# Kernel optimization log

Hardware: AMD Instinct MI355X
Metric: run time of the kernel (lower is better)

The kernel has to match this reference:

```python
import jax, jax.numpy as jnp
import numpy as np

S, N, C = 16384, 2048, 8  # n_samples, n_channels, n_components

def setup_inputs() -> dict:
    key = jax.random.key(0)
    k1, k2, k3, k4 = jax.random.split(key, 4)
    return {
        "inputs": jax.random.uniform(k1, (S, N), dtype=jnp.float32),
        "components": jax.random.uniform(k2, (C, N), dtype=jnp.float32),
        "contributions": jax.random.uniform(k3, (S, C), dtype=jnp.float32),
        "shift": jax.random.normal(k4, (S, C), dtype=jnp.float32) * 3.0,
    }

def reference(inputs, components, contributions, shift):
    # fit_shift=True branch. The original builds k_matrix[i,j] = j - i and
    # coeff[i,j] = clip(1 - |shift - (j - i)|, 0, 1), then dots with the
    # component. That is exactly linear interpolation of component at
    # position i + shift, with zero padding outside [0, N-1].
    n_samples, n_channels = inputs.shape
    n_comp = components.shape[0]
    i = jnp.arange(n_channels, dtype=shift.dtype)
    pos = i[None, None, :] + shift[:, :, None]            # [S, C, N]
    j0f = jnp.floor(pos)
    frac = pos - j0f                                      # in [0, 1)
    j0 = j0f.astype(jnp.int32)
    j1 = j0 + 1
    cidx = jnp.arange(n_comp)[None, :, None]              # broadcast over [S, C, N]
    g0 = components[cidx, jnp.clip(j0, 0, n_channels - 1)]
    g1 = components[cidx, jnp.clip(j1, 0, n_channels - 1)]
    v0 = ((j0 >= 0) & (j0 < n_channels)).astype(components.dtype)
    v1 = ((j1 >= 0) & (j1 < n_channels)).astype(components.dtype)
    shifted = g0 * (1.0 - frac) * v0 + g1 * frac * v1     # [S, C, N] shifted components
    # scale by per-sample contributions and sum over components
    return jnp.einsum('scn,sc->sn', shifted, contributions)
```

## Files before the change

kernel.cpp:

```cpp
#include <hip/hip_runtime.h>
#include <hip/hip_fp16.h>


namespace {
constexpr int kS     = 16384;
constexpr int kN     = 2048;
constexpr int kC     = 8;
constexpr int kM     = 16;
constexpr int kBlock = 256;
constexpr int kPadH  = 32;
constexpr int kUnits = 1057;
constexpr int kRowStride = 1192;

__device__ __forceinline__ int swz(int u) { return u + (u >> 3); }

__global__ __launch_bounds__(kBlock, 4)
void smf_kernel(const float* __restrict__ comps,
                const float* __restrict__ contrib,
                const float* __restrict__ shift,
                float* __restrict__ out)
{
    __shared__ uint32_t ldsU[kC * kRowStride];

    const int tid = threadIdx.x;

    for (int c = 0; c < kC; ++c) {
        const float* src = comps + c * kN;
        uint32_t* dst = ldsU + c * kRowStride;
        for (int u = tid; u < kUnits; u += kBlock) {
            const int j = 2 * u - kPadH;
            float2 v = make_float2(0.f, 0.f);
            if (j >= 0 && j < kN - 1) v = *reinterpret_cast<const float2*>(src + j);
            __half2 h2 = __floats2half2_rn(v.x, v.y);
            dst[swz(u)] = *reinterpret_cast<const uint32_t*>(&h2);
        }
    }
    __syncthreads();

    const int s0 = blockIdx.x * kM;
    const int n0 = tid * 8;

    float4 cA = *reinterpret_cast<const float4*>(contrib + (size_t)s0 * kC);
    float4 cB = *reinterpret_cast<const float4*>(contrib + (size_t)s0 * kC + 4);
    float4 sA = *reinterpret_cast<const float4*>(shift   + (size_t)s0 * kC);
    float4 sB = *reinterpret_cast<const float4*>(shift   + (size_t)s0 * kC + 4);

    #pragma unroll 1
    for (int si = 0; si < kM; ++si) {
        const int s = s0 + si;
        const float4 ccA = cA, ccB = cB, csA = sA, csB = sB;
        const int sn = (si + 1 < kM) ? (s + 1) : s;
        cA = *reinterpret_cast<const float4*>(contrib + (size_t)sn * kC);
        cB = *reinterpret_cast<const float4*>(contrib + (size_t)sn * kC + 4);
        sA = *reinterpret_cast<const float4*>(shift   + (size_t)sn * kC);
        sB = *reinterpret_cast<const float4*>(shift   + (size_t)sn * kC + 4);

        const float ct[8] = {ccA.x, ccA.y, ccA.z, ccA.w, ccB.x, ccB.y, ccB.z, ccB.w};
        const float sh[8] = {csA.x, csA.y, csA.z, csA.w, csB.x, csB.y, csB.z, csB.w};

        float acc[8];
        #pragma unroll
        for (int k = 0; k < 8; ++k) acc[k] = 0.f;

        #pragma unroll
        for (int c = 0; c < kC; ++c) {
            const float fl = floorf(sh[c]);
            const float fr = sh[c] - fl;
            int d = (int)fl;
            d = d < -31 ? -31 : (d > 31 ? 31 : d);
            const float w1 = ct[c] * fr;
            const float w0 = ct[c] - w1;

            const int a   = n0 + d + kPadH;
            const int u0  = a >> 1;
            const bool odd = (a & 1) != 0;

            const uint32_t* row = ldsU + c * kRowStride;
            const uint32_t y0 = row[swz(u0 + 0)];
            const uint32_t y1 = row[swz(u0 + 1)];
            const uint32_t y2 = row[swz(u0 + 2)];
            const uint32_t y3 = row[swz(u0 + 3)];
            const uint32_t y4 = row[swz(u0 + 4)];
            const uint32_t y5 = row[swz(u0 + 5)];

            const uint32_t z0 = odd ? __builtin_amdgcn_alignbit(y1, y0, 16) : y0;
            const uint32_t z1 = odd ? __builtin_amdgcn_alignbit(y2, y1, 16) : y1;
            const uint32_t z2 = odd ? __builtin_amdgcn_alignbit(y3, y2, 16) : y2;
            const uint32_t z3 = odd ? __builtin_amdgcn_alignbit(y4, y3, 16) : y3;
            const uint32_t z4 = odd ? __builtin_amdgcn_alignbit(y5, y4, 16) : y4;

            const float2 f0 = __half22float2(*reinterpret_cast<const __half2*>(&z0));
            const float2 f1 = __half22float2(*reinterpret_cast<const __half2*>(&z1));
            const float2 f2 = __half22float2(*reinterpret_cast<const __half2*>(&z2));
            const float2 f3 = __half22float2(*reinterpret_cast<const __half2*>(&z3));
            const float2 f4 = __half22float2(*reinterpret_cast<const __half2*>(&z4));

            acc[0] += w0 * f0.x + w1 * f0.y;
            acc[1] += w0 * f0.y + w1 * f1.x;
            acc[2] += w0 * f1.x + w1 * f1.y;
            acc[3] += w0 * f1.y + w1 * f2.x;
            acc[4] += w0 * f2.x + w1 * f2.y;
            acc[5] += w0 * f2.y + w1 * f3.x;
            acc[6] += w0 * f3.x + w1 * f3.y;
            acc[7] += w0 * f3.y + w1 * f4.x;
        }

        float4* orow = reinterpret_cast<float4*>(out + (size_t)s * kN + n0);
        orow[0] = make_float4(acc[0], acc[1], acc[2], acc[3]);
        orow[1] = make_float4(acc[4], acc[5], acc[6], acc[7]);
    }
}
}

extern "C" void kernel_launch(void* const* d_in, const int* in_sizes, int n_in,
                              void* d_out, int out_size, void* d_ws, size_t ws_size,
                              hipStream_t stream) {
    const float* comps   = (const float*)d_in[1];
    const float* contrib = (const float*)d_in[2];
    const float* shiftp  = (const float*)d_in[3];
    float* out = (float*)d_out;

    dim3 grid(kS / kM);
    dim3 block(kBlock);
    smf_kernel<<<grid, block, 0, stream>>>(comps, contrib, shiftp, out);
}
```

Measured before the change: 297.2 us.

## Use 1024-thread blocks over 32 samples and stage per-sample params in LDS

Blocks grow from 256 to 1024 threads, and each block now covers 32 samples split across four thread groups of 8 samples each. The per-sample contribution and shift vectors are loaded once into shared memory instead of being prefetched from global memory per iteration. The aim is to spread the fixed cost of converting the fp16 component table into LDS over twice as many output rows. The risk is that launch_bounds(1024, 8) limits registers per thread, which could cause spills. Fewer blocks also means coarser scheduling across CUs.

```diff
diff --git a/kernel.cpp b/kernel.cpp
--- a/kernel.cpp
+++ b/kernel.cpp
@@ -6,23 +6,26 @@
 constexpr int kS     = 16384;
 constexpr int kN     = 2048;
 constexpr int kC     = 8;
-constexpr int kM     = 16;
-constexpr int kBlock = 256;
+constexpr int kM     = 32;
+constexpr int kBlock = 1024;
 constexpr int kPadH  = 32;
 constexpr int kUnits = 1057;
 constexpr int kRowStride = 1192;
 
 __device__ __forceinline__ int swz(int u) { return u + (u >> 3); }
 
-__global__ __launch_bounds__(kBlock, 4)
+__global__ __launch_bounds__(kBlock, 8)
 void smf_kernel(const float* __restrict__ comps,
                 const float* __restrict__ contrib,
                 const float* __restrict__ shift,
                 float* __restrict__ out)
 {
     __shared__ uint32_t ldsU[kC * kRowStride];
+    __shared__ float    ctLds[kM * kC];
+    __shared__ float    shLds[kM * kC];
 
     const int tid = threadIdx.x;
+    const int s0  = blockIdx.x * kM;
 
     for (int c = 0; c < kC; ++c) {
         const float* src = comps + c * kN;
@@ -35,25 +38,31 @@
             dst[swz(u)] = *reinterpret_cast<const uint32_t*>(&h2);
         }
     }
+
+    for (int t = tid; t < (kM * kC) / 2; t += kBlock) {
+        if (t < (kM * kC) / 4) {
+            reinterpret_cast<float4*>(ctLds)[t] =
+                reinterpret_cast<const float4*>(contrib + (size_t)s0 * kC)[t];
+        } else {
+            const int t2 = t - (kM * kC) / 4;
+            reinterpret_cast<float4*>(shLds)[t2] =
+                reinterpret_cast<const float4*>(shift + (size_t)s0 * kC)[t2];
+        }
+    }
     __syncthreads();
 
-    const int s0 = blockIdx.x * kM;
-    const int n0 = tid * 8;
-
-    float4 cA = *reinterpret_cast<const float4*>(contrib + (size_t)s0 * kC);
-    float4 cB = *reinterpret_cast<const float4*>(contrib + (size_t)s0 * kC + 4);
-    float4 sA = *reinterpret_cast<const float4*>(shift   + (size_t)s0 * kC);
-    float4 sB = *reinterpret_cast<const float4*>(shift   + (size_t)s0 * kC + 4);
+    const int q  = tid >> 8;
+    const int n0 = (tid & 255) * 8;
 
     #pragma unroll 1
-    for (int si = 0; si < kM; ++si) {
-        const int s = s0 + si;
-        const float4 ccA = cA, ccB = cB, csA = sA, csB = sB;
-        const int sn = (si + 1 < kM) ? (s + 1) : s;
-        cA = *reinterpret_cast<const float4*>(contrib + (size_t)sn * kC);
-        cB = *reinterpret_cast<const float4*>(contrib + (size_t)sn * kC + 4);
-        sA = *reinterpret_cast<const float4*>(shift   + (size_t)sn * kC);
-        sB = *reinterpret_cast<const float4*>(shift   + (size_t)sn * kC + 4);
+    for (int r = 0; r < kM / 4; ++r) {
+        const int si = q * (kM / 4) + r;
+        const int s  = s0 + si;
+
+        const float4 ccA = *reinterpret_cast<const float4*>(ctLds + si * kC);
+        const float4 ccB = *reinterpret_cast<const float4*>(ctLds + si * kC + 4);
+        const float4 csA = *reinterpret_cast<const float4*>(shLds + si * kC);
+        const float4 csB = *reinterpret_cast<const float4*>(shLds + si * kC + 4);
 
         const float ct[8] = {ccA.x, ccA.y, ccA.z, ccA.w, ccB.x, ccB.y, ccB.z, ccB.w};
         const float sh[8] = {csA.x, csA.y, csA.z, csA.w, csB.x, csB.y, csB.z, csB.w};
```

Result: slower. 313.4 us (+5.4%).
